# Performance work log

Measured on AMD Instinct MI355X. Metric: run time of the kernel, lower is better.

The kernel has to match this reference:

```python
import jax, jax.numpy as jnp
import numpy as np

H = 128      # hidden_dim
HEADS = 4
HD = H // HEADS
B, S, D, A, I = 64, 512, 64, 3, 13


def layernorm(x, g, b, eps=1e-5):
    m = x.mean(-1, keepdims=True)
    v = ((x - m) ** 2).mean(-1, keepdims=True)
    return g * (x - m) / jnp.sqrt(v + eps) + b


def setup_inputs() -> dict:
    key = jax.random.key(0)
    ks = jax.random.split(key, 12)
    rn = lambda k, shp, s=0.05: jax.random.normal(k, shp, jnp.float32) * s
    return {
        "x": jax.random.normal(ks[0], (B, S, D), jnp.float32),
        "info": jax.random.normal(ks[1], (B, I), jnp.float32),
        "W_cell": rn(ks[2], (4 * H, D + H)), "b_cell": jnp.zeros(4 * H, jnp.float32),
        "Wqkv": rn(ks[3], (3 * H, H)), "bqkv": jnp.zeros(3 * H, jnp.float32),
        "Wo": rn(ks[4], (H, H)), "bo": jnp.zeros(H, jnp.float32),
        "ln_g": jnp.ones(H, jnp.float32), "ln_b": jnp.zeros(H, jnp.float32),
        "Wa1": rn(ks[5], (128, H + I)), "ba1": jnp.zeros(128, jnp.float32),
        "lna_g": jnp.ones(128, jnp.float32), "lna_b": jnp.zeros(128, jnp.float32),
        "Wa2": rn(ks[6], (A, 128)), "ba2": jnp.zeros(A, jnp.float32),
        "Wc1": rn(ks[7], (128, H + I)), "bc1": jnp.zeros(128, jnp.float32),
        "lnc_g": jnp.ones(128, jnp.float32), "lnc_b": jnp.zeros(128, jnp.float32),
        "Wc2": rn(ks[8], (1, 128)), "bc2": jnp.zeros(1, jnp.float32),
    }


def reference(x, info, W_cell, b_cell, Wqkv, bqkv, Wo, bo, ln_g, ln_b,
              Wa1, ba1, lna_g, lna_b, Wa2, ba2, Wc1, bc1, lnc_g, lnc_b, Wc2, bc2):
    Bx, Sx, _ = x.shape
    h0 = jnp.zeros((Bx, H), x.dtype)
    c0 = jnp.zeros((Bx, H), x.dtype)
    n0 = jnp.ones((Bx, H), x.dtype)

    def step(carry, xt):
        h, c, n = carry
        gates = jnp.concatenate([xt, h], -1) @ W_cell.T + b_cell
        i, f, o, z = jnp.split(gates, 4, axis=-1)
        i = jnp.exp(jnp.clip(i, -5.0, 5.0))
        f = jnp.exp(jnp.clip(f, -5.0, 5.0))
        c = jnp.clip(f * c + i * jnp.tanh(z), -1e6, 1e6)
        n = jnp.clip(f * n + i, 1e-6, 1e6)
        h = jnp.nan_to_num(jax.nn.sigmoid(o) * (c / n), nan=0.0, posinf=0.0, neginf=0.0)
        return (h, c, n), h

    _, hs = jax.lax.scan(step, (h0, c0, n0), jnp.swapaxes(x, 0, 1))  # (S,B,H)
    seq_h = jnp.swapaxes(hs, 0, 1)  # (B,S,H)

    # MultiheadAttention (self-attn, batch_first, shared in_proj)
    qkv = seq_h @ Wqkv.T + bqkv
    q, k, v = jnp.split(qkv, 3, -1)
    split_heads = lambda t: t.reshape(Bx, Sx, HEADS, HD).transpose(0, 2, 1, 3)
    q, k, v = split_heads(q), split_heads(k), split_heads(v)
    scores = jnp.einsum('bhqd,bhkd->bhqk', q, k) / np.sqrt(HD).astype(np.float32)
    attn = jax.nn.softmax(scores, axis=-1)
    av = jnp.einsum('bhqk,bhkd->bhqd', attn, v).transpose(0, 2, 1, 3).reshape(Bx, Sx, H)
    attn_out = av @ Wo.T + bo
    context = layernorm(seq_h + attn_out, ln_g, ln_b).mean(axis=1)  # (B,H)

    comb = jnp.concatenate([context, info], -1)  # (B, H+I)
    action_probs = jax.nn.softmax(
        jax.nn.relu(layernorm(comb @ Wa1.T + ba1, lna_g, lna_b)) @ Wa2.T + ba2, axis=-1)
    value = jax.nn.relu(layernorm(comb @ Wc1.T + bc1, lnc_g, lnc_b)) @ Wc2.T + bc2
    return (action_probs, value)
```

## Files before the change

kernel.cpp:

```cpp
#include <hip/hip_runtime.h>

typedef unsigned short ushort_t;
typedef unsigned int uint_t;

__device__ __forceinline__ float bflo(uint_t u){ union{uint_t i;float f;}v; v.i=u<<16; return v.f; }
__device__ __forceinline__ float bfhi(uint_t u){ union{uint_t i;float f;}v; v.i=u&0xffff0000u; return v.f; }
__device__ __forceinline__ float bfu(ushort_t u){ union{uint_t i;float f;}v; v.i=((uint_t)u)<<16; return v.f; }
__device__ __forceinline__ ushort_t f2b(float f){
  union{float f;uint_t i;}v; v.f=f;
  uint_t r = v.i + 0x7fffu + ((v.i>>16)&1u);
  return (ushort_t)(r>>16);
}
__device__ __forceinline__ void ld8bf(const ushort_t* p, float* w){
  uint4 u = *(const uint4*)p;
  w[0]=bflo(u.x); w[1]=bfhi(u.x); w[2]=bflo(u.y); w[3]=bfhi(u.y);
  w[4]=bflo(u.z); w[5]=bfhi(u.z); w[6]=bflo(u.w); w[7]=bfhi(u.w);
}
__device__ __forceinline__ void cvt8(uint4 u, float* d){
  d[0]=bflo(u.x); d[1]=bfhi(u.x); d[2]=bflo(u.y); d[3]=bfhi(u.y);
  d[4]=bflo(u.z); d[5]=bfhi(u.z); d[6]=bflo(u.w); d[7]=bfhi(u.w);
}
__device__ __forceinline__ float ldin(const void* p, size_t i, int isbf){
  return isbf ? bfu(((const ushort_t*)p)[i]) : ((const float*)p)[i];
}
__device__ __forceinline__ float rlane(float v, int l){
  return __uint_as_float(__builtin_amdgcn_readlane(__float_as_uint(v), l));
}
__device__ __forceinline__ int detect_bf(const void* lng){
  return (*(const uint_t*)lng == 0x3F803F80u) ? 1 : 0;
}

#define DOT128(acc, Wv, Bv) { float s0_=0.f,s1_=0.f,s2_=0.f,s3_=0.f; \
  _Pragma("unroll") \
  for (int k_=0;k_<128;k_+=4){ float4 h4_ = *(const float4*)&(Bv)[k_]; \
    s0_ += (Wv)[k_]*h4_.x; s1_ += (Wv)[k_+1]*h4_.y; \
    s2_ += (Wv)[k_+2]*h4_.z; s3_ += (Wv)[k_+3]*h4_.w; } \
  acc += (s0_+s1_)+(s2_+s3_); }
#define DOT64A(acc, Wv, Bv) { float s0_=0.f,s1_=0.f,s2_=0.f,s3_=0.f; \
  _Pragma("unroll") \
  for (int k_=0;k_<64;k_+=4){ float4 h4_ = *(const float4*)&(Bv)[k_]; \
    s0_ += (Wv)[k_]*h4_.x; s1_ += (Wv)[k_+1]*h4_.y; \
    s2_ += (Wv)[k_+2]*h4_.z; s3_ += (Wv)[k_+3]*h4_.w; } \
  acc += (s0_+s1_)+(s2_+s3_); }

typedef __attribute__((ext_vector_type(8))) short bf16x8;
typedef __attribute__((ext_vector_type(8))) _Float16 f16x8;
typedef __attribute__((ext_vector_type(4))) float f32x4;
__device__ __forceinline__ bf16x8 bcast8(uint4 u){ return __builtin_bit_cast(bf16x8, u); }
__device__ __forceinline__ f16x8  hcast8(uint4 u){ return __builtin_bit_cast(f16x8, u); }
__device__ __forceinline__ bf16x8 cvt8bf(const float* p){
  float4 a = *(const float4*)p; float4 b = *(const float4*)(p+4);
  uint4 u;
  u.x = (uint_t)f2b(a.x) | ((uint_t)f2b(a.y)<<16);
  u.y = (uint_t)f2b(a.z) | ((uint_t)f2b(a.w)<<16);
  u.z = (uint_t)f2b(b.x) | ((uint_t)f2b(b.y)<<16);
  u.w = (uint_t)f2b(b.z) | ((uint_t)f2b(b.w)<<16);
  return bcast8(u);
}
__device__ __forceinline__ void cvt8hl(const float* p, bf16x8* hi, bf16x8* lo){
  float v[8];
  *(float4*)&v[0] = *(const float4*)p;
  *(float4*)&v[4] = *(const float4*)(p+4);
  ushort_t h[8], l[8];
  #pragma unroll
  for (int j=0;j<8;++j){ h[j] = f2b(v[j]); l[j] = f2b(v[j] - bfu(h[j])); }
  uint4 uh = { (uint_t)h[0]|((uint_t)h[1]<<16), (uint_t)h[2]|((uint_t)h[3]<<16),
               (uint_t)h[4]|((uint_t)h[5]<<16), (uint_t)h[6]|((uint_t)h[7]<<16) };
  uint4 ul = { (uint_t)l[0]|((uint_t)l[1]<<16), (uint_t)l[2]|((uint_t)l[3]<<16),
               (uint_t)l[4]|((uint_t)l[5]<<16), (uint_t)l[6]|((uint_t)l[7]<<16) };
  *hi = bcast8(uh); *lo = bcast8(ul);
}
__device__ __forceinline__ ushort_t f2h(float f){
  _Float16 h = (_Float16)f;
  return __builtin_bit_cast(ushort_t, h);
}
__device__ __forceinline__ float h2f(ushort_t u){
  _Float16 h = __builtin_bit_cast(_Float16, u);
  return (float)h;
}

__global__ __launch_bounds__(256) void k_cvtw(const float* __restrict__ Wq,
    const float* __restrict__ Wo, const float* __restrict__ Wc,
    ushort_t* __restrict__ wqb, ushort_t* __restrict__ wob,
    ushort_t* __restrict__ wxh, ushort_t* __restrict__ wxl,
    ushort_t* __restrict__ whf, ushort_t* __restrict__ whl,
    const void* __restrict__ lng){
  if (detect_bf(lng)) return;
  int i = blockIdx.x*256 + threadIdx.x;
  if (i < 12288){
    float4 f = ((const float4*)Wq)[i];
    uint2 u = { (uint_t)f2b(f.x) | ((uint_t)f2b(f.y)<<16),
                (uint_t)f2b(f.z) | ((uint_t)f2b(f.w)<<16) };
    ((uint2*)wqb)[i] = u;
  } else if (i < 16384){
    int k = i - 12288;
    float4 f = ((const float4*)Wo)[k];
    uint2 u = { (uint_t)f2b(f.x) | ((uint_t)f2b(f.y)<<16),
                (uint_t)f2b(f.z) | ((uint_t)f2b(f.w)<<16) };
    ((uint2*)wob)[k] = u;
  } else if (i < 24576){
    int k = i - 16384;
    int j = k >> 4, kq = (k & 15)*4;
    float4 f = *(const float4*)(Wc + (size_t)j*192 + kq);
    ushort_t h0=f2b(f.x), h1=f2b(f.y), h2=f2b(f.z), h3=f2b(f.w);
    ushort_t l0=f2b(f.x-bfu(h0)), l1=f2b(f.y-bfu(h1));
    ushort_t l2=f2b(f.z-bfu(h2)), l3=f2b(f.w-bfu(h3));
    ((uint2*)(wxh + (size_t)j*64 + kq))[0] = { (uint_t)h0|((uint_t)h1<<16), (uint_t)h2|((uint_t)h3<<16) };
    ((uint2*)(wxl + (size_t)j*64 + kq))[0] = { (uint_t)l0|((uint_t)l1<<16), (uint_t)l2|((uint_t)l3<<16) };
  } else if (i < 32768){
    int k2 = i - 24576;
    int jp = k2 >> 4, kc = (k2 & 15)*8;
    int wvp = jp >> 6, g = (jp >> 4) & 3, l = jp & 15;
    int jorig = 128*g + 16*wvp + l;
    const float* src = Wc + (size_t)jorig*192 + 64 + kc;
    ushort_t hh[8], ll[8];
    #pragma unroll
    for (int q=0;q<8;++q){
      hh[q] = f2h(src[q]);
      ll[q] = f2h(src[q] - h2f(hh[q]));
    }
    uint4 uh = { (uint_t)hh[0]|((uint_t)hh[1]<<16), (uint_t)hh[2]|((uint_t)hh[3]<<16),
                 (uint_t)hh[4]|((uint_t)hh[5]<<16), (uint_t)hh[6]|((uint_t)hh[7]<<16) };
    uint4 ul = { (uint_t)ll[0]|((uint_t)ll[1]<<16), (uint_t)ll[2]|((uint_t)ll[3]<<16),
                 (uint_t)ll[4]|((uint_t)ll[5]<<16), (uint_t)ll[6]|((uint_t)ll[7]<<16) };
    *(uint4*)(whf + (size_t)jp*136 + kc) = uh;
    *(uint4*)(whl + (size_t)jp*128 + kc) = ul;
  }
}

__global__ __launch_bounds__(256) void k_gx_f32(const float* __restrict__ x,
    const float* __restrict__ bc,
    const ushort_t* __restrict__ wxh, const ushort_t* __restrict__ wxl,
    float* __restrict__ gx, const void* __restrict__ lng){
  if (detect_bf(lng)) return;
  int t = threadIdx.x, lane = t & 63, wave = t >> 6;
  int l16 = lane & 15, quad = lane >> 4;
  int rowb = blockIdx.x*64 + wave*16;
  const float* xp = x + (size_t)(rowb + l16)*64;
  bf16x8 xh0, xl0, xh1, xl1;
  cvt8hl(xp + quad*8,      &xh0, &xl0);
  cvt8hl(xp + 32 + quad*8, &xh1, &xl1);
  int r0 = rowb + quad*4;
  for (int ct=0; ct<32; ++ct){
    int j = ct*16 + l16;
    const ushort_t* bh = wxh + (size_t)j*64 + quad*8;
    const ushort_t* bl = wxl + (size_t)j*64 + quad*8;
    bf16x8 wh0 = bcast8(*(const uint4*)(bh));
    bf16x8 wh1 = bcast8(*(const uint4*)(bh + 32));
    bf16x8 wl0 = bcast8(*(const uint4*)(bl));
    bf16x8 wl1 = bcast8(*(const uint4*)(bl + 32));
    f32x4 acc = {0.f,0.f,0.f,0.f};
    acc = __builtin_amdgcn_mfma_f32_16x16x32_bf16(xh0, wh0, acc, 0,0,0);
    acc = __builtin_amdgcn_mfma_f32_16x16x32_bf16(xh1, wh1, acc, 0,0,0);
    acc = __builtin_amdgcn_mfma_f32_16x16x32_bf16(xh0, wl0, acc, 0,0,0);
    acc = __builtin_amdgcn_mfma_f32_16x16x32_bf16(xh1, wl1, acc, 0,0,0);
    acc = __builtin_amdgcn_mfma_f32_16x16x32_bf16(xl0, wh0, acc, 0,0,0);
    acc = __builtin_amdgcn_mfma_f32_16x16x32_bf16(xl1, wh1, acc, 0,0,0);
    float bj = bc[j];
    int dcol = ((j & 127) << 2) + (j >> 7);
    #pragma unroll
    for (int r=0;r<4;++r)
      gx[(size_t)(r0+r)*512 + dcol] = acc[r] + bj;
  }
}

__global__ __attribute__((amdgpu_flat_work_group_size(512,512), amdgpu_waves_per_eu(2,2)))
void k_rec_hl(const ushort_t* __restrict__ whf,
    const ushort_t* __restrict__ whl,
    const float* __restrict__ gx, float* __restrict__ seq_h,
    const void* __restrict__ lng){
  if (detect_bf(lng)) return;
  int b = blockIdx.x, t = threadIdx.x;
  int lane = t & 63, wv = t >> 6, l16 = lane & 15, quad = lane >> 4;
  __shared__ ushort_t wlds[512*136];
  __shared__ ushort_t hz[2][448];
  {
    const uint4* src = (const uint4*)whf;
    uint4* dst = (uint4*)wlds;
    for (int i=t; i<8704; i+=512) dst[i] = src[i];
  }
  if (t < 448){ hz[0][t] = (ushort_t)0; hz[1][t] = (ushort_t)0; }
  const float* gxb = gx + (size_t)b*512*512;
  const int hidx = 16*wv + l16;
  float c = 0.f, n = 1.f;
  const float* gxp = gxb + ((size_t)hidx << 2);
  float4 P0 = {0.f,0.f,0.f,0.f}, P1 = P0, P2 = P0, P3 = P0;
  if (quad == 0){
    P0 = *(const float4*)(gxp);
    P1 = *(const float4*)(gxp + 512);
    P2 = *(const float4*)(gxp + 1024);
    P3 = *(const float4*)(gxp + 1536);
  }
  float* shout = seq_h + (size_t)b*512*128;
  __syncthreads();
  const int c0 = 4*wv, c1 = 4*wv+1, c2 = 4*wv+2, c3 = 4*wv+3;
  const ushort_t* w0 = wlds + (c0*16 + l16)*136 + quad*8;
  const ushort_t* w1 = wlds + (c1*16 + l16)*136 + quad*8;
  const ushort_t* w2 = wlds + (c2*16 + l16)*136 + quad*8;
  const ushort_t* w3 = wlds + (c3*16 + l16)*136 + quad*8;
  const ushort_t* p0 = whl + (size_t)(c0*16 + l16)*128 + quad*8;
  const ushort_t* p1 = whl + (size_t)(c1*16 + l16)*128 + quad*8;
  const ushort_t* p2 = whl + (size_t)(c2*16 + l16)*128 + quad*8;
  const ushort_t* p3 = whl + (size_t)(c3*16 + l16)*128 + quad*8;
#define BDECL(T, ptr) uint4 T##0 = *(const uint4*)(ptr), T##1 = *(const uint4*)((ptr)+32), \
  T##2 = *(const uint4*)((ptr)+64), T##3 = *(const uint4*)((ptr)+96);
  BDECL(U0, w0) BDECL(U1, w1) BDECL(U2, w2) BDECL(U3, w3)
  BDECL(V0, p0) BDECL(V1, p1) BDECL(V2, p2) BDECL(V3, p3)
#undef BDECL
#define UPIN(U) asm volatile("" : "+v"(U.x), "+v"(U.y), "+v"(U.z), "+v"(U.w));
  UPIN(U00) UPIN(U01) UPIN(U02) UPIN(U03)
  UPIN(U10) UPIN(U11) UPIN(U12) UPIN(U13)
  UPIN(U20) UPIN(U21) UPIN(U22) UPIN(U23)
  UPIN(U30) UPIN(U31) UPIN(U32) UPIN(U33)
  UPIN(V00) UPIN(V01) UPIN(V02) UPIN(V03)
  UPIN(V10) UPIN(V11) UPIN(V12) UPIN(V13)
  UPIN(V20) UPIN(V21) UPIN(V22) UPIN(V23)
  UPIN(V30) UPIN(V31) UPIN(V32) UPIN(V33)
#undef UPIN
  const int hoff = ((l16 == 0) ? 0 : ((l16 == 1) ? 160 : 320)) + quad*8;
  const ushort_t* hzA = hz[0] + hoff;
  const ushort_t* hzB = hz[1] + hoff;
#define MFQU(AF, KK) \
    s0 = __builtin_amdgcn_mfma_f32_16x16x32_f16(AF, hcast8(U0##KK), s0, 0,0,0); \
    s1 = __builtin_amdgcn_mfma_f32_16x16x32_f16(AF, hcast8(U1##KK), s1, 0,0,0); \
    s2 = __builtin_amdgcn_mfma_f32_16x16x32_f16(AF, hcast8(U2##KK), s2, 0,0,0); \
    s3 = __builtin_amdgcn_mfma_f32_16x16x32_f16(AF, hcast8(U3##KK), s3, 0,0,0);
#define MFQV(AF, KK) \
    s0 = __builtin_amdgcn_mfma_f32_16x16x32_f16(AF, hcast8(V0##KK), s0, 0,0,0); \
    s1 = __builtin_amdgcn_mfma_f32_16x16x32_f16(AF, hcast8(V1##KK), s1, 0,0,0); \
    s2 = __builtin_amdgcn_mfma_f32_16x16x32_f16(AF, hcast8(V2##KK), s2, 0,0,0); \
    s3 = __builtin_amdgcn_mfma_f32_16x16x32_f16(AF, hcast8(V3##KK), s3, 0,0,0);
#define STEPBODY(TS, PAR, PS) { \
    const ushort_t* asrc = (PAR) ? hzB : hzA; \
    ushort_t* dstbuf = (PAR) ? hz[0] : hz[1]; \
    f16x8 A0 = hcast8(*(const uint4*)(asrc)); \
    f16x8 A1 = hcast8(*(const uint4*)(asrc + 32)); \
    f16x8 A2 = hcast8(*(const uint4*)(asrc + 64)); \
    f16x8 A3 = hcast8(*(const uint4*)(asrc + 96)); \
    f32x4 s0 = {0.f,0.f,0.f,0.f}, s1 = {0.f,0.f,0.f,0.f}; \
    f32x4 s2 = {0.f,0.f,0.f,0.f}, s3 = {0.f,0.f,0.f,0.f}; \
    MFQU(A0, 0) \
    MFQU(A1, 1) \
    MFQU(A2, 2) \
    MFQU(A3, 3) \
    MFQV(A0, 0) \
    MFQV(A1, 1) \
    MFQV(A2, 2) \
    MFQV(A3, 3) \
    if (quad == 0){ \
      float gi = s0[0] + s0[1] + PS.x; \
      float gf = s1[0] + s1[1] + PS.y; \
      float go = s2[0] + s2[1] + PS.z; \
      float gz = s3[0] + s3[1] + PS.w; \
      { int nts_ = (TS) + 4; if (nts_ >= 512) nts_ = 0; \
        PS = *(const float4*)(gxp + (size_t)nts_*512); } \
      float ii = __expf(fminf(fmaxf(gi,-5.f),5.f)); \
      float ff = __expf(fminf(fmaxf(gf,-5.f),5.f)); \
      float e2 = __expf(2.f*gz); \
      float zt = 1.f - 2.f/(e2+1.f); \
      c = fminf(fmaxf(ff*c + ii*zt, -1e6f), 1e6f); \
      n = fminf(fmaxf(ff*n + ii, 1e-6f), 1e6f); \
      float oo = 1.f/(1.f+__expf(-go)); \
      float h = oo*(c/n); \
      if (!isfinite(h)) h = 0.f; \
      shout[(size_t)(TS)*128 + hidx] = h; \
      ushort_t hhi = f2h(h); \
      dstbuf[hidx] = hhi; \
      dstbuf[160 + hidx] = f2h(h - h2f(hhi)); \
    } \
    asm volatile("s_waitcnt lgkmcnt(0)" ::: "memory"); \
    __builtin_amdgcn_s_barrier(); \
    asm volatile("" ::: "memory"); \
  }
  for (int ts=0; ts<512; ts+=4){
    STEPBODY(ts,   0, P0)
    STEPBODY(ts+1, 1, P1)
    STEPBODY(ts+2, 0, P2)
    STEPBODY(ts+3, 1, P3)
  }
#undef STEPBODY
#undef MFQU
#undef MFQV
}

__global__ __launch_bounds__(512) void k_rec_inl(const void* __restrict__ x,
    const void* __restrict__ Wc, const void* __restrict__ bc,
    float* __restrict__ seq_h, const void* __restrict__ lng, int only_bf){
  int isbf = detect_bf(lng);
  if (only_bf && !isbf) return;
  int b = blockIdx.x, j = threadIdx.x;
  __shared__ float hs[128];
  __shared__ float gs[512];
  __shared__ float xr[4][64];
  float w[128], wx[64];
  if (isbf){
    const ushort_t* wr = (const ushort_t*)Wc + (size_t)j*192;
    #pragma unroll
    for (int q=0;q<8;q++)  ld8bf(wr + 8*q, &wx[8*q]);
    #pragma unroll
    for (int q=0;q<16;q++) ld8bf(wr + 64 + 8*q, &w[8*q]);
  } else {
    const float* wr = (const float*)Wc + (size_t)j*192;
    #pragma unroll
    for (int q=0;q<16;q++){ float4 f=*(const float4*)(wr+4*q);
      wx[4*q]=f.x; wx[4*q+1]=f.y; wx[4*q+2]=f.z; wx[4*q+3]=f.w; }
    #pragma unroll
    for (int q=0;q<32;q++){ float4 f=*(const float4*)(wr+64+4*q);
      w[4*q]=f.x; w[4*q+1]=f.y; w[4*q+2]=f.z; w[4*q+3]=f.w; }
  }
  float bj = ldin(bc, j, isbf);
  float c = 0.f, n = 1.f;
  if (j < 128) hs[j] = 0.f;
  if (j < 128){
    int r = j>>6, k = j&63;
    xr[r][k] = ldin(x, ((size_t)b*512 + r)*64 + k, isbf);
  }
  __syncthreads();
  for (int t=0; t<512; ++t){
    const float* xt = xr[t&3];
    float acc = bj;
    DOT64A(acc, wx, xt);
    DOT128(acc, w, hs);
    gs[j] = acc;
    __syncthreads();
    if (j < 128){
      float gi=gs[j], gf=gs[128+j], go=gs[256+j], gz=gs[384+j];
      float ii = __expf(fminf(fmaxf(gi,-5.f),5.f));
      float ff = __expf(fminf(fmaxf(gf,-5.f),5.f));
      float e2 = __expf(2.f*gz);
      float zt = 1.f - 2.f/(e2+1.f);
      c = fminf(fmaxf(ff*c + ii*zt, -1e6f), 1e6f);
      n = fminf(fmaxf(ff*n + ii, 1e-6f), 1e6f);
      float oo = 1.f/(1.f+__expf(-go));
      float h = oo*(c/n);
      if (!isfinite(h)) h = 0.f;
      hs[j] = h;
      seq_h[((size_t)b*512 + t)*128 + j] = h;
    } else if (j >= 448 && (t+2) < 512){
      int k = j & 63;
      xr[(t+2)&3][k] = ldin(x, ((size_t)b*512 + (t+2))*64 + k, isbf);
    }
    __syncthreads();
  }
}

__global__ __launch_bounds__(256) void k_qkv(const float* __restrict__ seq_h,
    const void* __restrict__ Wq, const void* __restrict__ bq,
    const ushort_t* __restrict__ wqb,
    ushort_t* __restrict__ qkv, const void* __restrict__ lng){
  int isbf = detect_bf(lng);
  int row0 = blockIdx.x*32, t = threadIdx.x;
  if (isbf){
    __shared__ float hsb[4096];
    {
      const float4* hp = (const float4*)(seq_h + (size_t)row0*128);
      #pragma unroll
      for (int i=t;i<1024;i+=256) ((float4*)hsb)[i] = hp[i];
    }
    __syncthreads();
    for (int pass=0; pass<2; ++pass){
      int j = (pass==0) ? t : 256 + t;
      if (j >= 384) break;
      float w[128];
      const ushort_t* wr = (const ushort_t*)Wq + (size_t)j*128;
      #pragma unroll
      for (int q=0;q<16;q++) ld8bf(wr + 8*q, &w[8*q]);
      float bj = bfu(((const ushort_t*)bq)[j]);
      for (int s=0;s<32;++s){
        float acc = bj;
        DOT128(acc, w, &hsb[s*128]);
        qkv[(size_t)(row0+s)*384 + j] = f2b(acc);
      }
    }
  } else {
    int lane = t & 63, wave = t >> 6, l16 = lane & 15, quad = lane >> 4;
    int rt = wave & 1, chalf = wave >> 1;
    int rowg = row0 + rt*16 + l16;
    const float* hp = seq_h + (size_t)rowg*128 + quad*8;
    bf16x8 A0 = cvt8bf(hp);
    bf16x8 A1 = cvt8bf(hp + 32);
    bf16x8 A2 = cvt8bf(hp + 64);
    bf16x8 A3 = cvt8bf(hp + 96);
    int rbase = row0 + rt*16 + quad*4;
    for (int ci=0; ci<12; ++ci){
      int ct = chalf*12 + ci;
      int col = ct*16 + l16;
      const ushort_t* wb = wqb + (size_t)col*128 + quad*8;
      f32x4 acc = {0.f,0.f,0.f,0.f};
      acc = __builtin_amdgcn_mfma_f32_16x16x32_bf16(A0, bcast8(*(const uint4*)(wb)),      acc, 0,0,0);
      acc = __builtin_amdgcn_mfma_f32_16x16x32_bf16(A1, bcast8(*(const uint4*)(wb + 32)), acc, 0,0,0);
      acc = __builtin_amdgcn_mfma_f32_16x16x32_bf16(A2, bcast8(*(const uint4*)(wb + 64)), acc, 0,0,0);
      acc = __builtin_amdgcn_mfma_f32_16x16x32_bf16(A3, bcast8(*(const uint4*)(wb + 96)), acc, 0,0,0);
      float bj = ((const float*)bq)[col];
      #pragma unroll
      for (int r=0;r<4;++r)
        qkv[(size_t)(rbase+r)*384 + col] = f2b(acc[r] + bj);
    }
  }
}

#define AROW4(OP) OP(0) OP(1) OP(2) OP(3)
__global__ __launch_bounds__(512) void k_attn(const ushort_t* __restrict__ qkv,
    ushort_t* __restrict__ av){
  int b = blockIdx.x >> 2, h = blockIdx.x & 3;
  int t = threadIdx.x, lane = t & 63, wave = t >> 6;
  int l16 = lane & 15, quad = lane >> 4;
  __shared__ ushort_t Kt[512*40];
  __shared__ ushort_t Vt[32*520];
  __shared__ ushort_t Pl[8*16*72];
  const ushort_t* base = qkv + (size_t)b*512*384 + h*32;
  {
    const ushort_t* vr = base + (size_t)t*384 + 256;
    ushort_t tmp[32];
    *(uint4*)&tmp[0]  = *(const uint4*)(vr);
    *(uint4*)&tmp[8]  = *(const uint4*)(vr+8);
    *(uint4*)&tmp[16] = *(const uint4*)(vr+16);
    *(uint4*)&tmp[24] = *(const uint4*)(vr+24);
    #pragma unroll
    for (int d=0; d<32; ++d) Vt[d*520 + t] = tmp[d];
    const ushort_t* kr = base + (size_t)t*384 + 128;
    uint4 k0 = *(const uint4*)(kr);
    uint4 k1 = *(const uint4*)(kr+8);
    uint4 k2 = *(const uint4*)(kr+16);
    uint4 k3 = *(const uint4*)(kr+24);
    *(uint4*)&Kt[t*40]      = k0;
    *(uint4*)&Kt[t*40 + 8]  = k1;
    *(uint4*)&Kt[t*40 + 16] = k2;
    *(uint4*)&Kt[t*40 + 24] = k3;
  }
  __syncthreads();
  ushort_t* Pw = Pl + wave*16*72;
  const float scale = 0.17677669529663687f;
  for (int q4=0; q4<4; ++q4){
    int qt = wave + q4*8;
    bf16x8 qa;
    { uint4 u = *(const uint4*)(base + (size_t)(qt*16 + l16)*384 + quad*8);
      qa = bcast8(u); }
    f32x4 O0 = {0.f,0.f,0.f,0.f}, O1 = {0.f,0.f,0.f,0.f};
    float m0=-1e30f,m1=-1e30f,m2=-1e30f,m3=-1e30f;
    float l0=0.f,l1=0.f,l2=0.f,l3=0.f;
    for (int ch=0; ch<8; ++ch){
      f32x4 S0,S1,S2,S3;
      {
        uint4 u0 = *(const uint4*)&Kt[(ch*64 +  0 + l16)*40 + quad*8];
        uint4 u1 = *(const uint4*)&Kt[(ch*64 + 16 + l16)*40 + quad*8];
        uint4 u2 = *(const uint4*)&Kt[(ch*64 + 32 + l16)*40 + quad*8];
        uint4 u3 = *(const uint4*)&Kt[(ch*64 + 48 + l16)*40 + quad*8];
        f32x4 z = {0.f,0.f,0.f,0.f};
        S0 = __builtin_amdgcn_mfma_f32_16x16x32_bf16(qa, bcast8(u0), z, 0,0,0);
        S1 = __builtin_amdgcn_mfma_f32_16x16x32_bf16(qa, bcast8(u1), z, 0,0,0);
        S2 = __builtin_amdgcn_mfma_f32_16x16x32_bf16(qa, bcast8(u2), z, 0,0,0);
        S3 = __builtin_amdgcn_mfma_f32_16x16x32_bf16(qa, bcast8(u3), z, 0,0,0);
      }
#define CMAX(r) float c##r = fmaxf(fmaxf(S0[r],S1[r]), fmaxf(S2[r],S3[r])) * scale; \
      c##r = fmaxf(c##r, __shfl_xor(c##r,1)); c##r = fmaxf(c##r, __shfl_xor(c##r,2)); \
      c##r = fmaxf(c##r, __shfl_xor(c##r,4)); c##r = fmaxf(c##r, __shfl_xor(c##r,8)); \
      float M##r = fmaxf(m##r, c##r); float al##r = __expf(m##r - M##r); \
      m##r = M##r; O0[r] *= al##r; O1[r] *= al##r; l##r *= al##r;
      AROW4(CMAX)
#undef CMAX
#define PEXP(r) float ps##r; { \
      float p0 = __expf(S0[r]*scale - m##r); \
      float p1 = __expf(S1[r]*scale - m##r); \
      float p2 = __expf(S2[r]*scale - m##r); \
      float p3 = __expf(S3[r]*scale - m##r); \
      ps##r = (p0+p1)+(p2+p3); \
      Pw[(quad*4+(r))*72 +  0 + l16] = f2b(p0); \
      Pw[(quad*4+(r))*72 + 16 + l16] = f2b(p1); \
      Pw[(quad*4+(r))*72 + 32 + l16] = f2b(p2); \
      Pw[(quad*4+(r))*72 + 48 + l16] = f2b(p3); }
      AROW4(PEXP)
#undef PEXP
#define PSUM(r) ps##r += __shfl_xor(ps##r,1); ps##r += __shfl_xor(ps##r,2); \
      ps##r += __shfl_xor(ps##r,4); ps##r += __shfl_xor(ps##r,8); l##r += ps##r;
      AROW4(PSUM)
#undef PSUM
      asm volatile("s_waitcnt lgkmcnt(0)" ::: "memory");
      bf16x8 pa0, pa1;
      { uint4 u = *(const uint4*)&Pw[l16*72 + quad*8];      pa0 = bcast8(u); }
      { uint4 u = *(const uint4*)&Pw[l16*72 + 32 + quad*8]; pa1 = bcast8(u); }
      {
        uint4 v0 = *(const uint4*)&Vt[(l16)*520    + ch*64 + quad*8];
        uint4 v1 = *(const uint4*)&Vt[(l16)*520    + ch*64 + 32 + quad*8];
        uint4 v2 = *(const uint4*)&Vt[(16+l16)*520 + ch*64 + quad*8];
        uint4 v3 = *(const uint4*)&Vt[(16+l16)*520 + ch*64 + 32 + quad*8];
        O0 = __builtin_amdgcn_mfma_f32_16x16x32_bf16(pa0, bcast8(v0), O0, 0,0,0);
        O0 = __builtin_amdgcn_mfma_f32_16x16x32_bf16(pa1, bcast8(v1), O0, 0,0,0);
        O1 = __builtin_amdgcn_mfma_f32_16x16x32_bf16(pa0, bcast8(v2), O1, 0,0,0);
        O1 = __builtin_amdgcn_mfma_f32_16x16x32_bf16(pa1, bcast8(v3), O1, 0,0,0);
      }
    }
#define OST(r) { float iv = 1.f/l##r; int row = qt*16 + quad*4 + (r); \
      ushort_t* op = av + (size_t)(b*512 + row)*128 + h*32; \
      op[l16]      = f2b(O0[r]*iv); \
      op[16 + l16] = f2b(O1[r]*iv); }
    AROW4(OST)
#undef OST
  }
}

__global__ __launch_bounds__(256) void k_ctx(const ushort_t* __restrict__ av,
    const float* __restrict__ seq_h, const void* __restrict__ Wo,
    const void* __restrict__ bo_, const void* __restrict__ lng,
    const void* __restrict__ lnb, const ushort_t* __restrict__ wob,
    float* __restrict__ partial){
  int isbf = detect_bf(lng);
  __shared__ float rs[4096];
  __shared__ float mrow[32], srow[32];
  __shared__ float halfsum[128];
  int row0 = blockIdx.x*32, t = threadIdx.x;
  int j = t & 127, sh = t >> 7;
  if (isbf){
    __shared__ float avs[4096];
    {
      const uint4* ap = (const uint4*)(av + (size_t)row0*128);
      for (int i=t;i<512;i+=256) cvt8(ap[i], &avs[i*8]);
    }
    __syncthreads();
    float w[128];
    const ushort_t* wr = (const ushort_t*)Wo + (size_t)j*128;
    #pragma unroll
    for (int q=0;q<16;q++) ld8bf(wr + 8*q, &w[8*q]);
    float bj = bfu(((const ushort_t*)bo_)[j]);
    for (int si=0; si<16; ++si){
      int s = sh*16 + si;
      float acc = bj;
      DOT128(acc, w, &avs[s*128]);
      rs[s*128+j] = acc + seq_h[(size_t)(row0+s)*128 + j];
    }
  } else {
    int lane = t & 63, wave = t >> 6, l16 = lane & 15, quad = lane >> 4;
    int rt = wave & 1, chalf = wave >> 1;
    int rowg = row0 + rt*16 + l16;
    const ushort_t* ap = av + (size_t)rowg*128 + quad*8;
    bf16x8 A0 = bcast8(*(const uint4*)(ap));
    bf16x8 A1 = bcast8(*(const uint4*)(ap + 32));
    bf16x8 A2 = bcast8(*(const uint4*)(ap + 64));
    bf16x8 A3 = bcast8(*(const uint4*)(ap + 96));
    int rl0 = rt*16 + quad*4;
    for (int ci=0; ci<4; ++ci){
      int ct = chalf*4 + ci;
      int col = ct*16 + l16;
      const ushort_t* wb = wob + (size_t)col*128 + quad*8;
      f32x4 acc = {0.f,0.f,0.f,0.f};
      acc = __builtin_amdgcn_mfma_f32_16x16x32_bf16(A0, bcast8(*(const uint4*)(wb)),      acc, 0,0,0);
      acc = __builtin_amdgcn_mfma_f32_16x16x32_bf16(A1, bcast8(*(const uint4*)(wb + 32)), acc, 0,0,0);
      acc = __builtin_amdgcn_mfma_f32_16x16x32_bf16(A2, bcast8(*(const uint4*)(wb + 64)), acc, 0,0,0);
      acc = __builtin_amdgcn_mfma_f32_16x16x32_bf16(A3, bcast8(*(const uint4*)(wb + 96)), acc, 0,0,0);
      float bj2 = ((const float*)bo_)[col];
      #pragma unroll
      for (int r=0;r<4;++r){
        int rl = rl0 + r;
        rs[rl*128 + col] = acc[r] + bj2 + seq_h[(size_t)(row0+rl)*128 + col];
      }
    }
  }
  __syncthreads();
  {
    int rr = t>>3, part = t&7;
    float vals[16], sm = 0.f;
    #pragma unroll
    for (int k2=0;k2<16;k2++){ vals[k2] = rs[rr*128 + part + 8*k2]; sm += vals[k2]; }
    sm += __shfl_xor(sm,1); sm += __shfl_xor(sm,2); sm += __shfl_xor(sm,4);
    float mean = sm*(1.f/128.f);
    float vv = 0.f;
    #pragma unroll
    for (int k2=0;k2<16;k2++){ float d = vals[k2]-mean; vv += d*d; }
    vv += __shfl_xor(vv,1); vv += __shfl_xor(vv,2); vv += __shfl_xor(vv,4);
    if (part==0){ mrow[rr]=mean; srow[rr]=rsqrtf(vv*(1.f/128.f)+1e-5f); }
  }
  __syncthreads();
  float g = ldin(lng, j, isbf), bb = ldin(lnb, j, isbf);
  float accs = 0.f;
  for (int si=0; si<16; ++si){
    int s = sh*16 + si;
    accs += g*(rs[s*128+j]-mrow[s])*srow[s] + bb;
  }
  if (sh==0) halfsum[j] = accs;
  __syncthreads();
  if (sh==1){
    int bidx = row0>>9, tile = (row0>>5)&15;
    partial[((size_t)bidx*16 + tile)*128 + j] = halfsum[j] + accs;
  }
}

__global__ __launch_bounds__(128) void k_head(const float* __restrict__ partial,
    const void* __restrict__ info,
    const void* Wa1, const void* ba1, const void* lnag, const void* lnab,
    const void* Wa2, const void* ba2,
    const void* Wc1, const void* bc1, const void* lncg, const void* lncb,
    const void* Wc2, const void* bc2, void* __restrict__ out,
    const void* __restrict__ lng){
  int isbf = detect_bf(lng);
  int b = blockIdx.x, t = threadIdx.x;
  __shared__ float comb[144];
  __shared__ float red[128];
  __shared__ float uu[128];
  float s = 0.f;
  #pragma unroll
  for (int i=0;i<16;i++) s += partial[((size_t)b*16+i)*128 + t];
  comb[t] = s*(1.f/512.f);
  if (t < 13) comb[128+t] = ldin(info, (size_t)b*13+t, isbf);
  __syncthreads();
  for (int br=0; br<2; ++br){
    const void* W1 = br ? Wc1 : Wa1;
    const void* b1 = br ? bc1 : ba1;
    const void* lg_ = br ? lncg : lnag;
    const void* lb_ = br ? lncb : lnab;
    float a = ldin(b1, t, isbf);
    for (int k=0;k<141;k++) a += ldin(W1, (size_t)t*141+k, isbf)*comb[k];
    red[t] = a; __syncthreads();
    for (int st=64; st>0; st>>=1){ if (t<st) red[t]+=red[t+st]; __syncthreads(); }
    float mean = red[0]*(1.f/128.f);
    __syncthreads();
    float d = a - mean;
    red[t] = d*d; __syncthreads();
    for (int st=64; st>0; st>>=1){ if (t<st) red[t]+=red[t+st]; __syncthreads(); }
    float rstd = rsqrtf(red[0]*(1.f/128.f)+1e-5f);
    __syncthreads();
    float u = ldin(lg_, t, isbf)*d*rstd + ldin(lb_, t, isbf);
    uu[t] = fmaxf(u, 0.f);
    __syncthreads();
    if (br==0){
      if (t < 3){
        float lg2 = ldin(ba2, t, isbf);
        for (int k=0;k<128;k++) lg2 += ldin(Wa2, (size_t)t*128+k, isbf)*uu[k];
        red[t] = lg2;
      }
      __syncthreads();
      if (t==0){
        float mx = fmaxf(red[0], fmaxf(red[1], red[2]));
        float e0=__expf(red[0]-mx), e1=__expf(red[1]-mx), e2=__expf(red[2]-mx);
        float inv = 1.f/(e0+e1+e2);
        if (isbf){
          ushort_t* o = (ushort_t*)out;
          o[b*3+0]=f2b(e0*inv); o[b*3+1]=f2b(e1*inv); o[b*3+2]=f2b(e2*inv);
        } else {
          float* o = (float*)out;
          o[b*3+0]=e0*inv; o[b*3+1]=e1*inv; o[b*3+2]=e2*inv;
        }
      }
      __syncthreads();
    } else {
      if (t==0){
        float v = ldin(bc2, 0, isbf);
        for (int k=0;k<128;k++) v += ldin(Wc2, k, isbf)*uu[k];
        if (isbf) ((ushort_t*)out)[192 + b] = f2b(v);
        else      ((float*)out)[192 + b] = v;
      }
    }
  }
}

extern "C" void kernel_launch(void* const* d_in, const int* in_sizes, int n_in,
                              void* d_out, int out_size, void* d_ws, size_t ws_size,
                              hipStream_t stream){
  const void* x    = d_in[0];
  const void* info = d_in[1];
  const void* Wcell= d_in[2];
  const void* bcell= d_in[3];
  const void* Wqkv = d_in[4];
  const void* bqkv = d_in[5];
  const void* Wo   = d_in[6];
  const void* bo   = d_in[7];
  const void* lng  = d_in[8];
  const void* lnb  = d_in[9];
  const void* Wa1  = d_in[10];
  const void* ba1  = d_in[11];
  const void* lnag = d_in[12];
  const void* lnab = d_in[13];
  const void* Wa2  = d_in[14];
  const void* ba2  = d_in[15];
  const void* Wc1  = d_in[16];
  const void* bc1  = d_in[17];
  const void* lncg = d_in[18];
  const void* lncb = d_in[19];
  const void* Wc2  = d_in[20];
  const void* bc2  = d_in[21];

  char* ws = (char*)d_ws;
  const int bigws = (ws_size >= ((size_t)82<<20)) ? 1 : 0;
  float*    seqh = (float*)   ws;
  float*    gxf  = (float*)   (ws + ((size_t)16<<20));
  ushort_t* qkv  = (ushort_t*)(ws + ((size_t)16<<20));
  ushort_t* av   = (ushort_t*)(ws + ((size_t)40<<20));
  float*    part = (float*)   (ws + ((size_t)48<<20));
  ushort_t* wqb  = (ushort_t*)(ws + ((size_t)80<<20) + (1<<20));
  ushort_t* wob  = wqb + 384*128;
  ushort_t* wxh  = wob + 128*128;
  ushort_t* wxl  = wxh + 512*64;
  ushort_t* whf  = wxl + 512*64;
  ushort_t* whl  = whf + 512*136;

  if (bigws){
    k_cvtw  <<< 128, 256, 0, stream>>>((const float*)Wqkv, (const float*)Wo,
                                       (const float*)Wcell, wqb, wob, wxh, wxl, whf, whl, lng);
    k_gx_f32<<< 512, 256, 0, stream>>>((const float*)x, (const float*)bcell,
                                       wxh, wxl, gxf, lng);
    k_rec_inl<<<64, 512, 0, stream>>>(x, Wcell, bcell, seqh, lng, 1);
    k_rec_hl <<< 64,  512, 0, stream>>>(whf, whl, gxf, seqh, lng);
  } else {
    k_rec_inl<<<64, 512, 0, stream>>>(x, Wcell, bcell, seqh, lng, 0);
    k_cvtw  <<< 128, 256, 0, stream>>>((const float*)Wqkv, (const float*)Wo,
                                       (const float*)Wcell, wqb, wob, wxh, wxl, whf, whl, lng);
  }
  k_qkv <<<1024, 256, 0, stream>>>(seqh, Wqkv, bqkv, wqb, qkv, lng);
  k_attn<<< 256, 512, 0, stream>>>(qkv, av);
  k_ctx <<<1024, 256, 0, stream>>>(av, seqh, Wo, bo, lng, lnb, wob, part);
  k_head<<<  64, 128, 0, stream>>>(part, info, Wa1, ba1, lnag, lnab, Wa2, ba2,
                                   Wc1, bc1, lncg, lncb, Wc2, bc2, d_out, lng);
}
```

Before: 678.1 us.

## Compute transposed attention scores to keep P in registers, skipping LDS round-trip

The attention kernel now computes S^T by swapping the MFMA operands, so each lane holds the scores for one query row across keys. K rows are permuted in LDS so the resulting register layout matches the A-operand layout needed for the P·V MFMA. The probabilities can then be packed straight into bf16 operands, with no LDS write/read and no lgkmcnt wait. Softmax max and sum reductions drop from four per-row 16-lane shuffle chains to one value reduced across quads. The trade-off is extra __shfl calls to redistribute the rescale factors and the final 1/l to the output layout.

Result: faster. 654.6 us (-3.5%).

```diff
diff --git a/kernel.cpp b/kernel.cpp
--- a/kernel.cpp
+++ b/kernel.cpp
@@ -399,7 +399,6 @@
   }
 }
 
-#define AROW4(OP) OP(0) OP(1) OP(2) OP(3)
 __global__ __launch_bounds__(512) void k_attn(const ushort_t* __restrict__ qkv,
     ushort_t* __restrict__ av){
   int b = blockIdx.x >> 2, h = blockIdx.x & 3;
@@ -407,7 +406,6 @@
   int l16 = lane & 15, quad = lane >> 4;
   __shared__ ushort_t Kt[512*40];
   __shared__ ushort_t Vt[32*520];
-  __shared__ ushort_t Pl[8*16*72];
   const ushort_t* base = qkv + (size_t)b*512*384 + h*32;
   {
     const ushort_t* vr = base + (size_t)t*384 + 256;
@@ -418,18 +416,17 @@
     *(uint4*)&tmp[24] = *(const uint4*)(vr+24);
     #pragma unroll
     for (int d=0; d<32; ++d) Vt[d*520 + t] = tmp[d];
+    int kp = t & 63, chs = t >> 6;
+    int tt = ((kp>>2)&1) | ((kp>>5)<<1);
+    int ii = (((kp>>3)&3)<<2) | (kp&3);
+    int row = chs*64 + tt*16 + ii;
     const ushort_t* kr = base + (size_t)t*384 + 128;
-    uint4 k0 = *(const uint4*)(kr);
-    uint4 k1 = *(const uint4*)(kr+8);
-    uint4 k2 = *(const uint4*)(kr+16);
-    uint4 k3 = *(const uint4*)(kr+24);
-    *(uint4*)&Kt[t*40]      = k0;
-    *(uint4*)&Kt[t*40 + 8]  = k1;
-    *(uint4*)&Kt[t*40 + 16] = k2;
-    *(uint4*)&Kt[t*40 + 24] = k3;
+    *(uint4*)&Kt[row*40]      = *(const uint4*)(kr);
+    *(uint4*)&Kt[row*40 + 8]  = *(const uint4*)(kr+8);
+    *(uint4*)&Kt[row*40 + 16] = *(const uint4*)(kr+16);
+    *(uint4*)&Kt[row*40 + 24] = *(const uint4*)(kr+24);
   }
   __syncthreads();
-  ushort_t* Pw = Pl + wave*16*72;
   const float scale = 0.17677669529663687f;
   for (int q4=0; q4<4; ++q4){
     int qt = wave + q4*8;
@@ -437,8 +434,7 @@
     { uint4 u = *(const uint4*)(base + (size_t)(qt*16 + l16)*384 + quad*8);
       qa = bcast8(u); }
     f32x4 O0 = {0.f,0.f,0.f,0.f}, O1 = {0.f,0.f,0.f,0.f};
-    float m0=-1e30f,m1=-1e30f,m2=-1e30f,m3=-1e30f;
-    float l0=0.f,l1=0.f,l2=0.f,l3=0.f;
+    float m = -1e30f, l = 0.f;
     for (int ch=0; ch<8; ++ch){
       f32x4 S0,S1,S2,S3;
       {
@@ -447,39 +443,60 @@
         uint4 u2 = *(const uint4*)&Kt[(ch*64 + 32 + l16)*40 + quad*8];
         uint4 u3 = *(const uint4*)&Kt[(ch*64 + 48 + l16)*40 + quad*8];
         f32x4 z = {0.f,0.f,0.f,0.f};
-        S0 = __builtin_amdgcn_mfma_f32_16x16x32_bf16(qa, bcast8(u0), z, 0,0,0);
-        S1 = __builtin_amdgcn_mfma_f32_16x16x32_bf16(qa, bcast8(u1), z, 0,0,0);
-        S2 = __builtin_amdgcn_mfma_f32_16x16x32_bf16(qa, bcast8(u2), z, 0,0,0);
-        S3 = __builtin_amdgcn_mfma_f32_16x16x32_bf16(qa, bcast8(u3), z, 0,0,0);
-      }
-#define CMAX(r) float c##r = fmaxf(fmaxf(S0[r],S1[r]), fmaxf(S2[r],S3[r])) * scale; \
-      c##r = fmaxf(c##r, __shfl_xor(c##r,1)); c##r = fmaxf(c##r, __shfl_xor(c##r,2)); \
-      c##r = fmaxf(c##r, __shfl_xor(c##r,4)); c##r = fmaxf(c##r, __shfl_xor(c##r,8)); \
-      float M##r = fmaxf(m##r, c##r); float al##r = __expf(m##r - M##r); \
-      m##r = M##r; O0[r] *= al##r; O1[r] *= al##r; l##r *= al##r;
-      AROW4(CMAX)
-#undef CMAX
-#define PEXP(r) float ps##r; { \
-      float p0 = __expf(S0[r]*scale - m##r); \
-      float p1 = __expf(S1[r]*scale - m##r); \
-      float p2 = __expf(S2[r]*scale - m##r); \
-      float p3 = __expf(S3[r]*scale - m##r); \
-      ps##r = (p0+p1)+(p2+p3); \
-      Pw[(quad*4+(r))*72 +  0 + l16] = f2b(p0); \
-      Pw[(quad*4+(r))*72 + 16 + l16] = f2b(p1); \
-      Pw[(quad*4+(r))*72 + 32 + l16] = f2b(p2); \
-      Pw[(quad*4+(r))*72 + 48 + l16] = f2b(p3); }
-      AROW4(PEXP)
-#undef PEXP
-#define PSUM(r) ps##r += __shfl_xor(ps##r,1); ps##r += __shfl_xor(ps##r,2); \
-      ps##r += __shfl_xor(ps##r,4); ps##r += __shfl_xor(ps##r,8); l##r += ps##r;
-      AROW4(PSUM)
-#undef PSUM
-      asm volatile("s_waitcnt lgkmcnt(0)" ::: "memory");
-      bf16x8 pa0, pa1;
-      { uint4 u = *(const uint4*)&Pw[l16*72 + quad*8];      pa0 = bcast8(u); }
-      { uint4 u = *(const uint4*)&Pw[l16*72 + 32 + quad*8]; pa1 = bcast8(u); }
+        S0 = __builtin_amdgcn_mfma_f32_16x16x32_bf16(bcast8(u0), qa, z, 0,0,0);
+        S1 = __builtin_amdgcn_mfma_f32_16x16x32_bf16(bcast8(u1), qa, z, 0,0,0);
+        S2 = __builtin_amdgcn_mfma_f32_16x16x32_bf16(bcast8(u2), qa, z, 0,0,0);
+        S3 = __builtin_amdgcn_mfma_f32_16x16x32_bf16(bcast8(u3), qa, z, 0,0,0);
+      }
+      float mc;
       {
+        float a0 = fmaxf(fmaxf(S0[0],S0[1]), fmaxf(S0[2],S0[3]));
+        float a1 = fmaxf(fmaxf(S1[0],S1[1]), fmaxf(S1[2],S1[3]));
+        float a2 = fmaxf(fmaxf(S2[0],S2[1]), fmaxf(S2[2],S2[3]));
+        float a3 = fmaxf(fmaxf(S3[0],S3[1]), fmaxf(S3[2],S3[3]));
+        mc = fmaxf(fmaxf(a0,a1), fmaxf(a2,a3)) * scale;
+      }
+      mc = fmaxf(mc, __shfl_xor(mc,16));
+      mc = fmaxf(mc, __shfl_xor(mc,32));
+      float M = fmaxf(m, mc);
+      float al = __expf(m - M);
+      m = M;
+      l *= al;
+      {
+        float al0 = __shfl(al, quad*4+0);
+        float al1 = __shfl(al, quad*4+1);
+        float al2 = __shfl(al, quad*4+2);
+        float al3 = __shfl(al, quad*4+3);
+        O0[0]*=al0; O0[1]*=al1; O0[2]*=al2; O0[3]*=al3;
+        O1[0]*=al0; O1[1]*=al1; O1[2]*=al2; O1[3]*=al3;
+      }
+      float s_loc;
+      uint4 up0, up1;
+      {
+        float p00=__expf(S0[0]*scale-M), p01=__expf(S0[1]*scale-M);
+        float p02=__expf(S0[2]*scale-M), p03=__expf(S0[3]*scale-M);
+        float p10=__expf(S1[0]*scale-M), p11=__expf(S1[1]*scale-M);
+        float p12=__expf(S1[2]*scale-M), p13=__expf(S1[3]*scale-M);
+        float p20=__expf(S2[0]*scale-M), p21=__expf(S2[1]*scale-M);
+        float p22=__expf(S2[2]*scale-M), p23=__expf(S2[3]*scale-M);
+        float p30=__expf(S3[0]*scale-M), p31=__expf(S3[1]*scale-M);
+        float p32=__expf(S3[2]*scale-M), p33=__expf(S3[3]*scale-M);
+        s_loc = ((p00+p01)+(p02+p03)) + ((p10+p11)+(p12+p13))
+              + ((p20+p21)+(p22+p23)) + ((p30+p31)+(p32+p33));
+        up0.x = (uint_t)f2b(p00) | ((uint_t)f2b(p01)<<16);
+        up0.y = (uint_t)f2b(p02) | ((uint_t)f2b(p03)<<16);
+        up0.z = (uint_t)f2b(p10) | ((uint_t)f2b(p11)<<16);
+        up0.w = (uint_t)f2b(p12) | ((uint_t)f2b(p13)<<16);
+        up1.x = (uint_t)f2b(p20) | ((uint_t)f2b(p21)<<16);
+        up1.y = (uint_t)f2b(p22) | ((uint_t)f2b(p23)<<16);
+        up1.z = (uint_t)f2b(p30) | ((uint_t)f2b(p31)<<16);
+        up1.w = (uint_t)f2b(p32) | ((uint_t)f2b(p33)<<16);
+      }
+      s_loc += __shfl_xor(s_loc,16);
+      s_loc += __shfl_xor(s_loc,32);
+      l += s_loc;
+      {
+        bf16x8 pa0 = bcast8(up0), pa1 = bcast8(up1);
         uint4 v0 = *(const uint4*)&Vt[(l16)*520    + ch*64 + quad*8];
         uint4 v1 = *(const uint4*)&Vt[(l16)*520    + ch*64 + 32 + quad*8];
         uint4 v2 = *(const uint4*)&Vt[(16+l16)*520 + ch*64 + quad*8];
@@ -490,11 +507,16 @@
         O1 = __builtin_amdgcn_mfma_f32_16x16x32_bf16(pa1, bcast8(v3), O1, 0,0,0);
       }
     }
-#define OST(r) { float iv = 1.f/l##r; int row = qt*16 + quad*4 + (r); \
+    float iv = 1.f/l;
+    float iv0 = __shfl(iv, quad*4+0);
+    float iv1 = __shfl(iv, quad*4+1);
+    float iv2 = __shfl(iv, quad*4+2);
+    float iv3 = __shfl(iv, quad*4+3);
+#define OST(r, ivr) { int row = qt*16 + quad*4 + (r); \
       ushort_t* op = av + (size_t)(b*512 + row)*128 + h*32; \
-      op[l16]      = f2b(O0[r]*iv); \
-      op[16 + l16] = f2b(O1[r]*iv); }
-    AROW4(OST)
+      op[l16]      = f2b(O0[r]*(ivr)); \
+      op[16 + l16] = f2b(O1[r]*(ivr)); }
+    OST(0, iv0) OST(1, iv1) OST(2, iv2) OST(3, iv3)
 #undef OST
   }
 }
```
